# Performance work log

Measured on AMD Instinct MI355X. Metric: run time of the kernel, lower is better.

The kernel has to match this reference:

```python
import jax, jax.numpy as jnp
import numpy as np

B, N, C, K, RPE = 8, 4096, 256, 16, 64
LN_EPS = 1e-5


def _layernorm(x, g, b):
    m = jnp.mean(x, axis=-1, keepdims=True)
    v = jnp.mean((x - m) ** 2, axis=-1, keepdims=True)
    return (x - m) * jax.lax.rsqrt(v + LN_EPS) * g + b


def setup_inputs() -> dict:
    key = jax.random.key(0)
    ks = jax.random.split(key, 10)
    def w(k, shape, s=0.02):
        return jax.random.normal(k, shape, jnp.float32) * s
    return {
        "x": jax.random.normal(ks[0], (B, N, C), jnp.float32),
        "pos": jax.random.normal(ks[1], (B, N, 3), jnp.float32),
        "Wq": w(ks[2], (C, C)),
        "Wk": w(ks[3], (C, C)),
        "Wv": w(ks[4], (C, C)),
        "W1": w(ks[5], (3, RPE)), "b1": jnp.zeros((RPE,), jnp.float32),
        "W2": w(ks[6], (RPE, C)), "b2": jnp.zeros((C,), jnp.float32),
        "Wp": w(ks[7], (C, C)), "bp": jnp.zeros((C,), jnp.float32),
        "gq": jnp.ones((C,), jnp.float32), "betaq": jnp.zeros((C,), jnp.float32),
        "gkv": jnp.ones((C,), jnp.float32), "betakv": jnp.zeros((C,), jnp.float32),
    }


def reference(x, pos, Wq, Wk, Wv, W1, b1, W2, b2, Wp, bp, gq, betaq, gkv, betakv):
    scale = C ** (-0.5)
    x_q = _layernorm(x, gq, betaq)
    x_kv = _layernorm(x, gkv, betakv)
    q = x_q @ Wq                      # (B,N,C)
    k = x_kv @ Wk                     # (B,N,C)
    v = x_kv @ Wv                     # (B,N,C)

    # kNN over squared pairwise distances (self has distance 0 on the diagonal)
    a2 = jnp.sum(pos * pos, axis=-1)                       # (B,N)
    dist2 = a2[:, :, None] + a2[:, None, :] - 2.0 * jnp.einsum(
        "bnc,bmc->bnm", pos, pos)                          # (B,N,N)
    dist2 = jnp.maximum(dist2, 0.0)
    eye = jnp.eye(N, dtype=bool)
    dist2 = jnp.where(eye[None], 0.0, dist2)
    _, idx = jax.lax.top_k(-dist2, K)                      # (B,N,K) smallest-k

    gather = jax.vmap(lambda f, i: f[i])                   # (N,C),(N,K)->(N,K,C)
    k_nb = gather(k, idx)                                  # (B,N,K,C)
    v_nb = gather(v, idx)                                  # (B,N,K,C)
    pos_nb = gather(pos, idx)                              # (B,N,K,3)

    rel = pos[:, :, None, :] - pos_nb                      # (B,N,K,3)
    rel_enc = jax.nn.relu(rel @ W1 + b1) @ W2 + b2         # (B,N,K,C)

    attn_logits = jnp.einsum("bnc,bnkc->bnk", q, k_nb) * scale
    attn_logits = attn_logits + jnp.sum(rel_enc, axis=-1) * scale
    attn = jax.nn.softmax(attn_logits, axis=-1)            # (B,N,K)

    out = jnp.einsum("bnk,bnkc->bnc", attn, v_nb)
    out = out @ Wp + bp
    return out
```

## Files before the change

kernel.cpp:

```cpp
#include <hip/hip_runtime.h>
#include <hip/hip_bf16.h>
#include <stdint.h>

#define Bv 8
#define Nv 4096
#define Cv 256
#define Kv 16
#define RPEv 64
#define CAPv 160

typedef short bf16x8 __attribute__((ext_vector_type(8)));
typedef float f32x4 __attribute__((ext_vector_type(4)));
typedef _Float16 half2v __attribute__((ext_vector_type(2)));
typedef unsigned short u16x2 __attribute__((ext_vector_type(2)));

static __device__ __forceinline__ float bf2f(unsigned int u16) {
    union { unsigned int i; float f; } v; v.i = u16 << 16; return v.f;
}
static __device__ __forceinline__ unsigned short f2bf(float f) {
    union { float f; unsigned int i; } v; v.f = f;
    unsigned int x = v.i;
    return (unsigned short)((x + 0x7fffu + ((x >> 16) & 1u)) >> 16);
}
static __device__ __forceinline__ unsigned int umin32(unsigned int a, unsigned int b) { return a < b ? a : b; }
static __device__ __forceinline__ unsigned int umax32(unsigned int a, unsigned int b) { return a > b ? a : b; }
static __device__ __forceinline__ unsigned short f2h(float f) {
    _Float16 h = (_Float16)f; return __builtin_bit_cast(unsigned short, h);
}
static __device__ __forceinline__ float h2f(unsigned int u) {
    _Float16 h = __builtin_bit_cast(_Float16, (unsigned short)(u & 0xffffu)); return (float)h;
}
static __device__ __forceinline__ half2v bch2(unsigned int u) { return __builtin_bit_cast(half2v, u); }
static __device__ __forceinline__ unsigned int bcu32(u16x2 v) { return __builtin_bit_cast(unsigned int, v); }

__global__ __launch_bounds__(256) void pre_kernel(
    const float* __restrict__ x,
    const float* __restrict__ gq, const float* __restrict__ bq,
    const float* __restrict__ gkv, const float* __restrict__ bkv,
    unsigned short* __restrict__ Aq, unsigned short* __restrict__ Akv,
    const float* __restrict__ Wq, const float* __restrict__ Wk,
    const float* __restrict__ Wv, const float* __restrict__ Wp,
    unsigned short* __restrict__ Bt,
    const float* __restrict__ W2, const float* __restrict__ b2,
    float* __restrict__ w2sum, float* __restrict__ b2sum,
    const float* __restrict__ pos, char* __restrict__ ppos)
{
    const int bid = blockIdx.x;
    const int tid = threadIdx.x;
    if (bid < 4096) {
        const long r0 = (long)bid * 8;
        const int row = tid >> 5;
        const int c0 = (tid & 31) * 8;
        const float* xr = x + (r0 + row) * Cv + c0;
        float xv[8];
        *(float4*)&xv[0] = *(const float4*)xr;
        *(float4*)&xv[4] = *(const float4*)(xr + 4);
        float s = 0.f, s2 = 0.f;
#pragma unroll
        for (int i = 0; i < 8; ++i) { s += xv[i]; s2 = fmaf(xv[i], xv[i], s2); }
#pragma unroll
        for (int m = 16; m >= 1; m >>= 1) { s += __shfl_xor(s, m); s2 += __shfl_xor(s2, m); }
        const float mean = s * (1.f / Cv);
        const float var = fmaf(-mean, mean, s2 * (1.f / Cv));
        const float rs = rsqrtf(fmaxf(var, 0.f) + 1e-5f);
        unsigned int pq[4], pk[4];
#pragma unroll
        for (int i = 0; i < 4; ++i) {
            const int c = c0 + 2 * i;
            const float h0 = (xv[2 * i] - mean) * rs;
            const float h1 = (xv[2 * i + 1] - mean) * rs;
            const unsigned int q0 = f2bf(fmaf(h0, gq[c], bq[c]));
            const unsigned int q1 = f2bf(fmaf(h1, gq[c + 1], bq[c + 1]));
            const unsigned int k0 = f2bf(fmaf(h0, gkv[c], bkv[c]));
            const unsigned int k1 = f2bf(fmaf(h1, gkv[c + 1], bkv[c + 1]));
            pq[i] = q0 | (q1 << 16);
            pk[i] = k0 | (k1 << 16);
        }
        const long off = (r0 + row) * Cv + c0;
        *(uint4*)&Aq[off]  = make_uint4(pq[0], pq[1], pq[2], pq[3]);
        *(uint4*)&Akv[off] = make_uint4(pk[0], pk[1], pk[2], pk[3]);
    } else if (bid < 5120) {
        const int r = bid - 4096;
        const float* W = (r < 256) ? Wq : (r < 512) ? Wk : (r < 768) ? Wv : Wp;
        const int n = r & 255;
        Bt[r * 256 + tid] = f2bf(W[tid * 256 + n]);
    } else if (bid == 5120) {
        if (tid < RPEv) {
            float s = 0.f;
            for (int c = 0; c < Cv; ++c) s += W2[tid * Cv + c];
            w2sum[tid] = s;
        }
        if (tid == 0) {
            float s = 0.f;
            for (int c = 0; c < Cv; ++c) s += b2[c];
            *b2sum = s;
        }
    } else {
        const int b = bid - 5121;
        const float* pb = pos + (size_t)b * Nv * 3;
        uint2* oxy = (uint2*)(ppos + (size_t)b * 24576);
        unsigned int* oz = (unsigned int*)(ppos + (size_t)b * 24576 + 16384);
        for (int i = tid; i < Nv / 2; i += 256) {
            const float* pp = pb + 6 * i;
            const float2 u0 = *(const float2*)pp;
            const float2 u1 = *(const float2*)(pp + 2);
            const float2 u2 = *(const float2*)(pp + 4);
            const unsigned int x0 = f2h(u0.x), y0 = f2h(u0.y), z0 = f2h(u1.x);
            const unsigned int x1 = f2h(u1.y), y1 = f2h(u2.x), z1 = f2h(u2.y);
            oxy[i] = make_uint2(x0 | (x1 << 16), y0 | (y1 << 16));
            oz[i] = z0 | (z1 << 16);
        }
    }
}

__global__ __launch_bounds__(256) void gemm_qkv_kernel(
    const unsigned short* __restrict__ Aq, const unsigned short* __restrict__ Akv,
    const unsigned short* __restrict__ Bt,
    unsigned short* __restrict__ qo, unsigned short* __restrict__ ko,
    unsigned short* __restrict__ vo)
{
    __shared__ unsigned short Albs[2][128 * 64];
    __shared__ unsigned short Blbs[2][128 * 64];

    const int tid = threadIdx.x;
    const int rt = blockIdx.x;
    const int ct = blockIdx.y;
    const unsigned short* A = (ct < 2) ? Aq : Akv;
    const int mat = ct >> 1;
    unsigned short* outp = (mat == 0) ? qo : (mat == 1) ? ko : vo;
    const int colInMat = (ct & 1) * 128;

    const int wid = tid >> 6, l = tid & 63;
    const int wr = wid >> 1, wc = wid & 1;

    int srow[4], scol8[4];
#pragma unroll
    for (int it = 0; it < 4; ++it) {
        const int chunk = it * 256 + tid;
        srow[it] = chunk >> 3;
        scol8[it] = ((chunk & 7) ^ (srow[it] & 7)) * 8;
    }

#define STAGE(buf, ks)                                                                  \
    {                                                                                   \
        _Pragma("unroll")                                                               \
        for (int it = 0; it < 4; ++it) {                                                \
            const unsigned short* ga = A + ((size_t)(rt * 128 + srow[it])) * 256        \
                                         + (ks) * 64 + scol8[it];                       \
            const unsigned short* gb = Bt + ((size_t)(ct * 128 + srow[it])) * 256       \
                                          + (ks) * 64 + scol8[it];                      \
            __builtin_amdgcn_global_load_lds(                                           \
                (const __attribute__((address_space(1))) unsigned int*)(const void*)ga, \
                (__attribute__((address_space(3))) unsigned int*)(void*)                \
                    ((char*)&Albs[buf][0] + (it * 256 + tid) * 16), 16, 0, 0);          \
            __builtin_amdgcn_global_load_lds(                                           \
                (const __attribute__((address_space(1))) unsigned int*)(const void*)gb, \
                (__attribute__((address_space(3))) unsigned int*)(void*)                \
                    ((char*)&Blbs[buf][0] + (it * 256 + tid) * 16), 16, 0, 0);          \
        }                                                                               \
    }

    f32x4 acc[4][4];
#pragma unroll
    for (int m = 0; m < 4; ++m)
#pragma unroll
        for (int n = 0; n < 4; ++n) acc[m][n] = (f32x4){0.f, 0.f, 0.f, 0.f};

    STAGE(0, 0);
    __syncthreads();

    for (int ks = 0; ks < 4; ++ks) {
        const int cur = ks & 1;
        if (ks < 3) STAGE(cur ^ 1, ks + 1);
#pragma unroll
        for (int kk = 0; kk < 2; ++kk) {
            bf16x8 a[4], b[4];
#pragma unroll
            for (int m = 0; m < 4; ++m) {
                const int row = wr * 64 + m * 16 + (l & 15);
                const int byte = row * 128 + ((((kk * 4 + (l >> 4)) * 16)) ^ ((row & 7) << 4));
                a[m] = *(const bf16x8*)((const char*)&Albs[cur][0] + byte);
            }
#pragma unroll
            for (int n = 0; n < 4; ++n) {
                const int row = wc * 64 + n * 16 + (l & 15);
                const int byte = row * 128 + ((((kk * 4 + (l >> 4)) * 16)) ^ ((row & 7) << 4));
                b[n] = *(const bf16x8*)((const char*)&Blbs[cur][0] + byte);
            }
#pragma unroll
            for (int m = 0; m < 4; ++m)
#pragma unroll
                for (int n = 0; n < 4; ++n)
                    acc[m][n] = __builtin_amdgcn_mfma_f32_16x16x32_bf16(a[m], b[n], acc[m][n], 0, 0, 0);
        }
        __syncthreads();
    }

#pragma unroll
    for (int m = 0; m < 4; ++m) {
#pragma unroll
        for (int n = 0; n < 4; ++n) {
#pragma unroll
            for (int j = 0; j < 4; ++j) {
                const int row = rt * 128 + wr * 64 + m * 16 + (l >> 4) * 4 + j;
                const int col = colInMat + wc * 64 + n * 16 + (l & 15);
                outp[(size_t)row * 256 + col] = f2bf(acc[m][n][j]);
            }
        }
    }
#undef STAGE
}

__global__ __launch_bounds__(256) void gemm_proj_kernel(
    const unsigned short* __restrict__ Ab, const unsigned short* __restrict__ Btp,
    const float* __restrict__ bp, float* __restrict__ out)
{
    __shared__ unsigned short Albs[2][128 * 64];
    __shared__ unsigned short Blbs[2][128 * 64];

    const int tid = threadIdx.x;
    const int rt = blockIdx.x;
    const int ct = blockIdx.y;

    const int wid = tid >> 6, l = tid & 63;
    const int wr = wid >> 1, wc = wid & 1;

    int srow[4], scol8[4];
#pragma unroll
    for (int it = 0; it < 4; ++it) {
        const int chunk = it * 256 + tid;
        srow[it] = chunk >> 3;
        scol8[it] = ((chunk & 7) ^ (srow[it] & 7)) * 8;
    }

#define STAGE(buf, ks)                                                                  \
    {                                                                                   \
        _Pragma("unroll")                                                               \
        for (int it = 0; it < 4; ++it) {                                                \
            const unsigned short* ga = Ab + ((size_t)(rt * 128 + srow[it])) * 256       \
                                          + (ks) * 64 + scol8[it];                      \
            const unsigned short* gb = Btp + ((size_t)(ct * 128 + srow[it])) * 256      \
                                           + (ks) * 64 + scol8[it];                     \
            __builtin_amdgcn_global_load_lds(                                           \
                (const __attribute__((address_space(1))) unsigned int*)(const void*)ga, \
                (__attribute__((address_space(3))) unsigned int*)(void*)                \
                    ((char*)&Albs[buf][0] + (it * 256 + tid) * 16), 16, 0, 0);          \
            __builtin_amdgcn_global_load_lds(                                           \
                (const __attribute__((address_space(1))) unsigned int*)(const void*)gb, \
                (__attribute__((address_space(3))) unsigned int*)(void*)                \
                    ((char*)&Blbs[buf][0] + (it * 256 + tid) * 16), 16, 0, 0);          \
        }                                                                               \
    }

    f32x4 acc[4][4];
#pragma unroll
    for (int m = 0; m < 4; ++m)
#pragma unroll
        for (int n = 0; n < 4; ++n) acc[m][n] = (f32x4){0.f, 0.f, 0.f, 0.f};

    STAGE(0, 0);
    __syncthreads();

    for (int ks = 0; ks < 4; ++ks) {
        const int cur = ks & 1;
        if (ks < 3) STAGE(cur ^ 1, ks + 1);
#pragma unroll
        for (int kk = 0; kk < 2; ++kk) {
            bf16x8 a[4], b[4];
#pragma unroll
            for (int m = 0; m < 4; ++m) {
                const int row = wr * 64 + m * 16 + (l & 15);
                const int byte = row * 128 + ((((kk * 4 + (l >> 4)) * 16)) ^ ((row & 7) << 4));
                a[m] = *(const bf16x8*)((const char*)&Albs[cur][0] + byte);
            }
#pragma unroll
            for (int n = 0; n < 4; ++n) {
                const int row = wc * 64 + n * 16 + (l & 15);
                const int byte = row * 128 + ((((kk * 4 + (l >> 4)) * 16)) ^ ((row & 7) << 4));
                b[n] = *(const bf16x8*)((const char*)&Blbs[cur][0] + byte);
            }
#pragma unroll
            for (int m = 0; m < 4; ++m)
#pragma unroll
                for (int n = 0; n < 4; ++n)
                    acc[m][n] = __builtin_amdgcn_mfma_f32_16x16x32_bf16(a[m], b[n], acc[m][n], 0, 0, 0);
        }
        __syncthreads();
    }

#pragma unroll
    for (int n = 0; n < 4; ++n) {
        const int col = ct * 128 + wc * 64 + n * 16 + (l & 15);
        const float bpv = bp[col];
#pragma unroll
        for (int m = 0; m < 4; ++m) {
#pragma unroll
            for (int j = 0; j < 4; ++j) {
                const int row = rt * 128 + wr * 64 + m * 16 + (l >> 4) * 4 + j;
                out[(size_t)row * 256 + col] = acc[m][n][j] + bpv;
            }
        }
    }
#undef STAGE
}

__global__ __launch_bounds__(256) void knn_kernel(
    const float* __restrict__ pos, const char* __restrict__ ppos,
    int* __restrict__ idx_out)
{
    __shared__ char Pbuf[24576];
    __shared__ uint4 qu[32];
    __shared__ unsigned int akeys[256 * 3];
    __shared__ unsigned int cnt[32];
    __shared__ unsigned short bufs[32 * CAPv];

    const uint2* pxy2 = (const uint2*)Pbuf;
    const unsigned int* pz2 = (const unsigned int*)(Pbuf + 16384);

    const int tid = threadIdx.x;
    const int ql = tid >> 3;
    const int s  = tid & 7;
    const int q  = blockIdx.x * 32 + ql;
    const int b  = q >> 12;
    const int n  = q & (Nv - 1);

    {
        const char* src = ppos + (size_t)b * 24576;
#pragma unroll
        for (int it = 0; it < 6; ++it) {
            const int off = (it * 256 + tid) * 16;
            __builtin_amdgcn_global_load_lds(
                (const __attribute__((address_space(1))) unsigned int*)(const void*)(src + off),
                (__attribute__((address_space(3))) unsigned int*)(void*)(Pbuf + off),
                16, 0, 0);
        }
    }
    __syncthreads();

    const int pq = n >> 1;
    const int hq = (n & 1) * 16;
    const uint2 qxy = pxy2[pq];
    const unsigned int qzz = pz2[pq];
    const unsigned int hx = (qxy.x >> hq) & 0xffffu;
    const unsigned int hy = (qxy.y >> hq) & 0xffffu;
    const unsigned int hz = (qzz   >> hq) & 0xffffu;
    const half2v qxp = bch2(hx | (hx << 16));
    const half2v qyp = bch2(hy | (hy << 16));
    const half2v qzp = bch2(hz | (hz << 16));

    u16x2 ch0 = {0x7c00, 0x7c00}, ch1 = ch0, ch2 = ch0;
    for (int t = 0; t < 128; ++t) {
        const int p = 8 * t + s;
        const uint2 xy = pxy2[p];
        const unsigned int zz = pz2[p];
        const half2v dx = bch2(xy.x) - qxp;
        const half2v dy = bch2(xy.y) - qyp;
        const half2v dz = bch2(zz) - qzp;
        const half2v d2 = dx * dx + dy * dy + dz * dz;
        const u16x2 k = __builtin_bit_cast(u16x2, d2);
        const u16x2 mn0 = __builtin_elementwise_min(ch0, k);
        const u16x2 mx0 = __builtin_elementwise_max(ch0, k);
        ch0 = mn0;
        const u16x2 mn1 = __builtin_elementwise_min(ch1, mx0);
        const u16x2 mx1 = __builtin_elementwise_max(ch1, mx0);
        ch1 = mn1;
        ch2 = __builtin_elementwise_min(ch2, mx1);
    }
    akeys[tid * 3 + 0] = bcu32(ch0);
    akeys[tid * 3 + 1] = bcu32(ch1);
    akeys[tid * 3 + 2] = bcu32(ch2);
    __syncthreads();

    if (tid < 32) {
        unsigned int sel16[16];
#pragma unroll
        for (int i = 0; i < 16; ++i) sel16[i] = 0xFFFFFFFFu;
        for (int s8 = 0; s8 < 8; ++s8) {
#pragma unroll
            for (int i3 = 0; i3 < 3; ++i3) {
                const unsigned int v = akeys[(8 * tid + s8) * 3 + i3];
#pragma unroll
                for (int h = 0; h < 2; ++h) {
                    unsigned int cand = (h == 0) ? (v & 0xffffu) : (v >> 16);
                    if (cand < sel16[15]) {
#pragma unroll
                        for (int i = 0; i < 16; ++i) {
                            const unsigned int lo = umin32(sel16[i], cand);
                            cand = umax32(sel16[i], cand);
                            sel16[i] = lo;
                        }
                    }
                }
            }
        }
        const float tauf = h2f(sel16[15]) * 1.12f + 1e-9f;
        const unsigned int taub = f2h(tauf);
        const int n2 = (blockIdx.x * 32 + tid) & (Nv - 1);
        const int pq2 = n2 >> 1;
        const int hq2 = (n2 & 1) * 16;
        const uint2 qxy2 = pxy2[pq2];
        const unsigned int qzz2 = pz2[pq2];
        const unsigned int hx2 = (qxy2.x >> hq2) & 0xffffu;
        const unsigned int hy2 = (qxy2.y >> hq2) & 0xffffu;
        const unsigned int hz2 = (qzz2   >> hq2) & 0xffffu;
        qu[tid] = make_uint4(hx2 | (hx2 << 16), hy2 | (hy2 << 16),
                             hz2 | (hz2 << 16), taub);
        cnt[tid] = 0;
    }
    __syncthreads();

    uint2 cxy[8]; unsigned int czp[8];
#pragma unroll
    for (int k = 0; k < 8; ++k) {
        cxy[k] = pxy2[tid + (k << 8)];
        czp[k] = pz2[tid + (k << 8)];
    }
    for (int q2 = 0; q2 < 32; ++q2) {
        const uint4 Q = qu[q2];
        const half2v Qx = bch2(Q.x), Qy = bch2(Q.y), Qz = bch2(Q.z);
        const unsigned int taub = Q.w;
#pragma unroll
        for (int k = 0; k < 8; ++k) {
            const half2v dx = bch2(cxy[k].x) - Qx;
            const half2v dy = bch2(cxy[k].y) - Qy;
            const half2v dz = bch2(czp[k]) - Qz;
            const half2v d2 = dx * dx + dy * dy + dz * dz;
            const unsigned int bits = __builtin_bit_cast(unsigned int, d2);
            const unsigned int lo = bits & 0xffffu;
            const unsigned int hi = bits >> 16;
            const int p = tid + (k << 8);
            if (lo < taub) {
                const unsigned int slot = atomicAdd(&cnt[q2], 1u);
                if (slot < CAPv) bufs[q2 * CAPv + slot] = (unsigned short)(2 * p);
            }
            if (hi < taub) {
                const unsigned int slot = atomicAdd(&cnt[q2], 1u);
                if (slot < CAPv) bufs[q2 * CAPv + slot] = (unsigned short)(2 * p + 1);
            }
        }
    }
    __syncthreads();

    if (tid < 32) {
        const int q2 = blockIdx.x * 32 + tid;
        const int n2 = q2 & (Nv - 1);
        const int b2 = q2 >> 12;
        const float* pb2 = pos + (size_t)b2 * Nv * 3;
        const double qxd = (double)pb2[3 * n2];
        const double qyd = (double)pb2[3 * n2 + 1];
        const double qzd = (double)pb2[3 * n2 + 2];
        const double a2qd = qxd * qxd + qyd * qyd + qzd * qzd;
        int c = (int)cnt[tid]; if (c > CAPv) c = CAPv;
        unsigned long long sel[Kv];
#pragma unroll
        for (int i = 0; i < Kv; ++i) sel[i] = ~0ull;
        for (int t = 0; t < c; ++t) {
            const int j = bufs[tid * CAPv + t];
            const double cxd = (double)pb2[3 * j];
            const double cyd = (double)pb2[3 * j + 1];
            const double czd = (double)pb2[3 * j + 2];
            const double a2cd = cxd * cxd + cyd * cyd + czd * czd;
            const double ddot = qxd * cxd + qyd * cyd + qzd * czd;
            double dv = (a2qd + a2cd) - 2.0 * ddot;
            dv = (dv < 0.0) ? 0.0 : dv;
            if (j == n2) dv = 0.0;
            union { double d; unsigned long long u; } cv; cv.d = dv;
            const unsigned long long key = (cv.u & ~0xFFFULL) | (unsigned long long)j;
            if (key < sel[Kv - 1]) {
                unsigned long long cc = key;
#pragma unroll
                for (int i = 0; i < Kv; ++i) {
                    const unsigned long long lo = (sel[i] < cc) ? sel[i] : cc;
                    const unsigned long long hi = (sel[i] < cc) ? cc : sel[i];
                    sel[i] = lo; cc = hi;
                }
            }
        }
#pragma unroll
        for (int i = 0; i < Kv; ++i)
            idx_out[(long)q2 * Kv + i] = (int)(sel[i] & 0xFFFull);
    }
}

__global__ __launch_bounds__(256) void attn_core_kernel(
    unsigned short* __restrict__ qb, const unsigned short* __restrict__ kb,
    const unsigned short* __restrict__ vb, const int* __restrict__ idx,
    const float* __restrict__ pos, const float* __restrict__ W1,
    const float* __restrict__ b1, const float* __restrict__ w2sum,
    const float* __restrict__ b2sum)
{
    __shared__ float q_lds[8][Cv];
    __shared__ float lg[8][Kv];
    __shared__ float wgt[8][Kv];
    __shared__ int idx_l[8][Kv];
    __shared__ float W1l[3 * RPEv];
    __shared__ float b1l[RPEv], w2s[RPEv];
    __shared__ float posq[24];
    __shared__ float b2s_l;

    const int tid = threadIdx.x;
    const long r0 = (long)blockIdx.x * 8;
    const int bq = (int)(r0 >> 12);

    {
        float* ql = &q_lds[0][0];
        for (int i = tid; i < 8 * Cv; i += 256) ql[i] = bf2f(qb[r0 * Cv + i]);
    }
    if (tid < 128) ((int*)idx_l)[tid] = idx[r0 * Kv + tid];
    if (tid < 3 * RPEv) W1l[tid] = W1[tid];
    if (tid < RPEv) { b1l[tid] = b1[tid]; w2s[tid] = w2sum[tid]; }
    if (tid < 24) posq[tid] = pos[r0 * 3 + tid];
    if (tid == 0) b2s_l = *b2sum;
    __syncthreads();

    const int g = tid >> 4, l = tid & 15;
    for (int r = 0; r < 8; ++r) {
        const int nb = idx_l[r][g];
        const long gi = (long)bq * Nv + nb;
        const unsigned short* kr = kb + gi * Cv + l * 16;
        const float* qq = &q_lds[r][l * 16];
        const uint4 kA = *(const uint4*)kr;
        const uint4 kB = *(const uint4*)(kr + 8);
        float part = 0.f;
        part = fmaf(qq[0],  bf2f(kA.x & 0xffffu), part);
        part = fmaf(qq[1],  bf2f(kA.x >> 16),     part);
        part = fmaf(qq[2],  bf2f(kA.y & 0xffffu), part);
        part = fmaf(qq[3],  bf2f(kA.y >> 16),     part);
        part = fmaf(qq[4],  bf2f(kA.z & 0xffffu), part);
        part = fmaf(qq[5],  bf2f(kA.z >> 16),     part);
        part = fmaf(qq[6],  bf2f(kA.w & 0xffffu), part);
        part = fmaf(qq[7],  bf2f(kA.w >> 16),     part);
        part = fmaf(qq[8],  bf2f(kB.x & 0xffffu), part);
        part = fmaf(qq[9],  bf2f(kB.x >> 16),     part);
        part = fmaf(qq[10], bf2f(kB.y & 0xffffu), part);
        part = fmaf(qq[11], bf2f(kB.y >> 16),     part);
        part = fmaf(qq[12], bf2f(kB.z & 0xffffu), part);
        part = fmaf(qq[13], bf2f(kB.z >> 16),     part);
        part = fmaf(qq[14], bf2f(kB.w & 0xffffu), part);
        part = fmaf(qq[15], bf2f(kB.w >> 16),     part);
        const float rx = posq[r * 3 + 0] - pos[gi * 3 + 0];
        const float ry = posq[r * 3 + 1] - pos[gi * 3 + 1];
        const float rz = posq[r * 3 + 2] - pos[gi * 3 + 2];
#pragma unroll
        for (int u4 = 0; u4 < 4; ++u4) {
            const int u = l * 4 + u4;
            float h = fmaf(rx, W1l[u], fmaf(ry, W1l[RPEv + u], fmaf(rz, W1l[2 * RPEv + u], b1l[u])));
            h = fmaxf(h, 0.f);
            part = fmaf(h, w2s[u], part);
        }
        part += __shfl_xor(part, 8);
        part += __shfl_xor(part, 4);
        part += __shfl_xor(part, 2);
        part += __shfl_xor(part, 1);
        if (l == 0) lg[r][g] = (part + b2s_l) * 0.0625f;
    }
    __syncthreads();
    if (tid < 128) {
        const int rr = tid >> 4, gg = tid & 15;
        const float v = lg[rr][gg];
        float m = v;
        m = fmaxf(m, __shfl_xor(m, 8)); m = fmaxf(m, __shfl_xor(m, 4));
        m = fmaxf(m, __shfl_xor(m, 2)); m = fmaxf(m, __shfl_xor(m, 1));
        const float e = __expf(v - m);
        float ssum = e;
        ssum += __shfl_xor(ssum, 8); ssum += __shfl_xor(ssum, 4);
        ssum += __shfl_xor(ssum, 2); ssum += __shfl_xor(ssum, 1);
        wgt[rr][gg] = e / ssum;
    }
    __syncthreads();
    {
        const int c = tid;
        for (int r = 0; r < 8; ++r) {
            float acc = 0.f;
#pragma unroll
            for (int t = 0; t < Kv; ++t) {
                const long gi = (long)bq * Nv + idx_l[r][t];
                acc = fmaf(wgt[r][t], bf2f((unsigned)vb[gi * Cv + c]), acc);
            }
            qb[(r0 + r) * Cv + c] = f2bf(acc);
        }
    }
}

extern "C" void kernel_launch(void* const* d_in, const int* in_sizes, int n_in,
                              void* d_out, int out_size, void* d_ws, size_t ws_size,
                              hipStream_t stream) {
    (void)in_sizes; (void)n_in; (void)out_size; (void)ws_size;
    const float* x      = (const float*)d_in[0];
    const float* pos    = (const float*)d_in[1];
    const float* Wq     = (const float*)d_in[2];
    const float* Wk     = (const float*)d_in[3];
    const float* Wv     = (const float*)d_in[4];
    const float* W1     = (const float*)d_in[5];
    const float* b1     = (const float*)d_in[6];
    const float* W2     = (const float*)d_in[7];
    const float* b2     = (const float*)d_in[8];
    const float* Wp     = (const float*)d_in[9];
    const float* bp     = (const float*)d_in[10];
    const float* gq     = (const float*)d_in[11];
    const float* betaq  = (const float*)d_in[12];
    const float* gkv    = (const float*)d_in[13];
    const float* betakv = (const float*)d_in[14];
    float* out = (float*)d_out;

    char* ws = (char*)d_ws;
    unsigned short* qb = (unsigned short*)(ws);
    unsigned short* kb = (unsigned short*)(ws + 16777216);
    unsigned short* vb = (unsigned short*)(ws + 33554432);
    int*   idx   = (int*)  (ws + 50331648);
    unsigned short* Bt = (unsigned short*)(ws + 52428800);
    float* w2sum = (float*)(ws + 52953088);
    float* b2sum = (float*)(ws + 52953344);
    char*  ppos  = ws + 52953600;

    unsigned short* Aq  = (unsigned short*)d_out;
    unsigned short* Akv = (unsigned short*)d_out + 8388608;

    hipLaunchKernelGGL(pre_kernel, dim3(5129), dim3(256), 0, stream,
                       x, gq, betaq, gkv, betakv, Aq, Akv,
                       Wq, Wk, Wv, Wp, Bt, W2, b2, w2sum, b2sum, pos, ppos);
    hipLaunchKernelGGL(gemm_qkv_kernel, dim3(256, 6), dim3(256), 0, stream,
                       Aq, Akv, Bt, qb, kb, vb);
    hipLaunchKernelGGL(knn_kernel, dim3(1024), dim3(256), 0, stream, pos, ppos, idx);
    hipLaunchKernelGGL(attn_core_kernel, dim3(4096), dim3(256), 0, stream,
                       qb, kb, vb, idx, pos, W1, b1, w2sum, b2sum);
    hipLaunchKernelGGL(gemm_proj_kernel, dim3(256, 2), dim3(256), 0, stream,
                       qb, Bt + 768 * 256, bp, out);
}
```

Measured before the change: 222.0 us.

## Split kNN into tau, MFMA-based candidate filter, and fp64 select kernels

The monolithic kNN kernel becomes four kernels. A build kernel packs positions into split-bf16 16-wide vectors so squared distance is computed with MFMA dot products. A tau kernel computes per-query thresholds, a filter kernel runs the MFMA distance pass with atomic candidate buffering, and a select kernel does the exact fp64 top-k over candidates with one thread per query instead of 32 threads per block. This moves the brute-force distance work from packed-half VALU to matrix cores and spreads the serial selection across all threads, at the cost of extra launches and global round-trips for candidate buffers. Split-bf16 precision could let through more or different candidates than the half-precision path did.

```diff
diff --git a/kernel.cpp b/kernel.cpp
--- a/kernel.cpp
+++ b/kernel.cpp
@@ -304,23 +304,18 @@
 #undef STAGE
 }
 
-__global__ __launch_bounds__(256) void knn_kernel(
-    const float* __restrict__ pos, const char* __restrict__ ppos,
-    int* __restrict__ idx_out)
+__global__ __launch_bounds__(256) void ktau_kernel(
+    const char* __restrict__ ppos, float* __restrict__ tau_g)
 {
     __shared__ char Pbuf[24576];
-    __shared__ uint4 qu[32];
     __shared__ unsigned int akeys[256 * 3];
-    __shared__ unsigned int cnt[32];
-    __shared__ unsigned short bufs[32 * CAPv];
 
     const uint2* pxy2 = (const uint2*)Pbuf;
     const unsigned int* pz2 = (const unsigned int*)(Pbuf + 16384);
 
     const int tid = threadIdx.x;
-    const int ql = tid >> 3;
     const int s  = tid & 7;
-    const int q  = blockIdx.x * 32 + ql;
+    const int q  = blockIdx.x * 32 + (tid >> 3);
     const int b  = q >> 12;
     const int n  = q & (Nv - 1);
 
@@ -393,93 +388,155 @@
                 }
             }
         }
-        const float tauf = h2f(sel16[15]) * 1.12f + 1e-9f;
-        const unsigned int taub = f2h(tauf);
-        const int n2 = (blockIdx.x * 32 + tid) & (Nv - 1);
-        const int pq2 = n2 >> 1;
-        const int hq2 = (n2 & 1) * 16;
-        const uint2 qxy2 = pxy2[pq2];
-        const unsigned int qzz2 = pz2[pq2];
-        const unsigned int hx2 = (qxy2.x >> hq2) & 0xffffu;
-        const unsigned int hy2 = (qxy2.y >> hq2) & 0xffffu;
-        const unsigned int hz2 = (qzz2   >> hq2) & 0xffffu;
-        qu[tid] = make_uint4(hx2 | (hx2 << 16), hy2 | (hy2 << 16),
-                             hz2 | (hz2 << 16), taub);
-        cnt[tid] = 0;
-    }
-    __syncthreads();
-
-    uint2 cxy[8]; unsigned int czp[8];
-#pragma unroll
-    for (int k = 0; k < 8; ++k) {
-        cxy[k] = pxy2[tid + (k << 8)];
-        czp[k] = pz2[tid + (k << 8)];
-    }
-    for (int q2 = 0; q2 < 32; ++q2) {
-        const uint4 Q = qu[q2];
-        const half2v Qx = bch2(Q.x), Qy = bch2(Q.y), Qz = bch2(Q.z);
-        const unsigned int taub = Q.w;
-#pragma unroll
-        for (int k = 0; k < 8; ++k) {
-            const half2v dx = bch2(cxy[k].x) - Qx;
-            const half2v dy = bch2(cxy[k].y) - Qy;
-            const half2v dz = bch2(czp[k]) - Qz;
-            const half2v d2 = dx * dx + dy * dy + dz * dz;
-            const unsigned int bits = __builtin_bit_cast(unsigned int, d2);
-            const unsigned int lo = bits & 0xffffu;
-            const unsigned int hi = bits >> 16;
-            const int p = tid + (k << 8);
-            if (lo < taub) {
-                const unsigned int slot = atomicAdd(&cnt[q2], 1u);
-                if (slot < CAPv) bufs[q2 * CAPv + slot] = (unsigned short)(2 * p);
-            }
-            if (hi < taub) {
-                const unsigned int slot = atomicAdd(&cnt[q2], 1u);
-                if (slot < CAPv) bufs[q2 * CAPv + slot] = (unsigned short)(2 * p + 1);
-            }
-        }
-    }
-    __syncthreads();
-
-    if (tid < 32) {
-        const int q2 = blockIdx.x * 32 + tid;
-        const int n2 = q2 & (Nv - 1);
-        const int b2 = q2 >> 12;
-        const float* pb2 = pos + (size_t)b2 * Nv * 3;
-        const double qxd = (double)pb2[3 * n2];
-        const double qyd = (double)pb2[3 * n2 + 1];
-        const double qzd = (double)pb2[3 * n2 + 2];
-        const double a2qd = qxd * qxd + qyd * qyd + qzd * qzd;
-        int c = (int)cnt[tid]; if (c > CAPv) c = CAPv;
-        unsigned long long sel[Kv];
-#pragma unroll
-        for (int i = 0; i < Kv; ++i) sel[i] = ~0ull;
-        for (int t = 0; t < c; ++t) {
-            const int j = bufs[tid * CAPv + t];
-            const double cxd = (double)pb2[3 * j];
-            const double cyd = (double)pb2[3 * j + 1];
-            const double czd = (double)pb2[3 * j + 2];
-            const double a2cd = cxd * cxd + cyd * cyd + czd * czd;
-            const double ddot = qxd * cxd + qyd * cyd + qzd * czd;
-            double dv = (a2qd + a2cd) - 2.0 * ddot;
-            dv = (dv < 0.0) ? 0.0 : dv;
-            if (j == n2) dv = 0.0;
-            union { double d; unsigned long long u; } cv; cv.d = dv;
-            const unsigned long long key = (cv.u & ~0xFFFULL) | (unsigned long long)j;
-            if (key < sel[Kv - 1]) {
-                unsigned long long cc = key;
-#pragma unroll
-                for (int i = 0; i < Kv; ++i) {
-                    const unsigned long long lo = (sel[i] < cc) ? sel[i] : cc;
-                    const unsigned long long hi = (sel[i] < cc) ? cc : sel[i];
-                    sel[i] = lo; cc = hi;
+        tau_g[blockIdx.x * 32 + tid] = h2f(sel16[15]) * 1.12f + 1e-9f;
+    }
+}
+
+__global__ __launch_bounds__(256) void build16_kernel(
+    const float* __restrict__ pos,
+    unsigned short* __restrict__ Aq16g, unsigned short* __restrict__ Bq16g)
+{
+    const int t = blockIdx.x * 256 + threadIdx.x;
+    const float px = pos[3 * t], py = pos[3 * t + 1], pz = pos[3 * t + 2];
+    unsigned short ah[3], al[3], m2h[3], m2l[3];
+    const float c[3] = {px, py, pz};
+#pragma unroll
+    for (int i = 0; i < 3; ++i) {
+        ah[i] = f2bf(c[i]);
+        const float hi = bf2f(ah[i]);
+        al[i] = f2bf(c[i] - hi);
+        m2h[i] = f2bf(-2.f * hi);
+        m2l[i] = f2bf(-2.f * bf2f(al[i]));
+    }
+    const float sA = fmaf(px, px, fmaf(py, py, pz * pz));
+    const unsigned short sh = f2bf(sA);
+    const unsigned short sl = f2bf(sA - bf2f(sh));
+    const unsigned short one = 0x3F80;
+
+    unsigned short a16[16] = {ah[0], ah[1], ah[2], al[0], al[1], al[2],
+                              ah[0], ah[1], ah[2], al[0], al[1], al[2],
+                              sh, sl, one, one};
+    unsigned short b16[16] = {m2h[0], m2h[1], m2h[2], m2h[0], m2h[1], m2h[2],
+                              m2l[0], m2l[1], m2l[2], m2l[0], m2l[1], m2l[2],
+                              one, one, sh, sl};
+    uint4* ao = (uint4*)(Aq16g + (size_t)t * 16);
+    uint4* bo = (uint4*)(Bq16g + (size_t)t * 16);
+    ao[0] = *(uint4*)&a16[0]; ao[1] = *(uint4*)&a16[8];
+    bo[0] = *(uint4*)&b16[0]; bo[1] = *(uint4*)&b16[8];
+}
+
+__global__ __launch_bounds__(256) void kfilter_kernel(
+    const unsigned short* __restrict__ Aq16g, const unsigned short* __restrict__ Bq16g,
+    const float* __restrict__ tau_g, unsigned int* __restrict__ gcnt,
+    unsigned short* __restrict__ gbufs)
+{
+    __shared__ unsigned short Bst[1024 * 16];
+    __shared__ unsigned short Ast[64 * 16];
+    __shared__ unsigned short bufsL[64 * CAPv];
+    __shared__ unsigned int cntL[64];
+    __shared__ float tauL[64];
+
+    const int tid = threadIdx.x;
+    const int qb0 = blockIdx.x * 64;
+    const int batch = qb0 >> 12;
+    const int wave = tid >> 6;
+    const int l = tid & 63;
+    const int kc = l >> 4;
+
+    if (tid < 128) {
+        __builtin_amdgcn_global_load_lds(
+            (const __attribute__((address_space(1))) unsigned int*)(const void*)
+                ((const char*)Aq16g + (size_t)qb0 * 32 + tid * 16),
+            (__attribute__((address_space(3))) unsigned int*)(void*)((char*)Ast + tid * 16),
+            16, 0, 0);
+    }
+    if (tid < 64) { tauL[tid] = tau_g[qb0 + tid]; cntL[tid] = 0; }
+    __syncthreads();
+
+    const bf16x8 z8 = (bf16x8){0, 0, 0, 0, 0, 0, 0, 0};
+    bf16x8 afr = z8;
+    if (kc < 2) afr = *(const bf16x8*)(Ast + (wave * 16 + (l & 15)) * 16 + kc * 8);
+    float tr[4];
+#pragma unroll
+    for (int j = 0; j < 4; ++j) tr[j] = tauL[wave * 16 + (l >> 4) * 4 + j];
+
+    for (int chunk = 0; chunk < 4; ++chunk) {
+#pragma unroll
+        for (int it = 0; it < 8; ++it) {
+            __builtin_amdgcn_global_load_lds(
+                (const __attribute__((address_space(1))) unsigned int*)(const void*)
+                    ((const char*)Bq16g + ((size_t)batch * 4096 + chunk * 1024) * 32
+                     + (it * 256 + tid) * 16),
+                (__attribute__((address_space(3))) unsigned int*)(void*)
+                    ((char*)Bst + (it * 256 + tid) * 16),
+                16, 0, 0);
+        }
+        __syncthreads();
+        for (int nt = 0; nt < 64; ++nt) {
+            bf16x8 bfr = z8;
+            if (kc < 2) bfr = *(const bf16x8*)(Bst + (nt * 16 + (l & 15)) * 16 + kc * 8);
+            const f32x4 acc = __builtin_amdgcn_mfma_f32_16x16x32_bf16(
+                afr, bfr, (f32x4){0.f, 0.f, 0.f, 0.f}, 0, 0, 0);
+            const int cand = chunk * 1024 + nt * 16 + (l & 15);
+#pragma unroll
+            for (int j = 0; j < 4; ++j) {
+                if (acc[j] < tr[j]) {
+                    const int rl = wave * 16 + (l >> 4) * 4 + j;
+                    const unsigned int slot = atomicAdd(&cntL[rl], 1u);
+                    if (slot < CAPv) bufsL[rl * CAPv + slot] = (unsigned short)cand;
                 }
             }
         }
-#pragma unroll
-        for (int i = 0; i < Kv; ++i)
-            idx_out[(long)q2 * Kv + i] = (int)(sel[i] & 0xFFFull);
-    }
+        __syncthreads();
+    }
+
+    if (tid < 64) gcnt[qb0 + tid] = umin32(cntL[tid], CAPv);
+    for (int i = tid; i < 64 * CAPv; i += 256)
+        gbufs[(size_t)qb0 * CAPv + i] = bufsL[i];
+}
+
+__global__ __launch_bounds__(256) void kselect_kernel(
+    const float* __restrict__ pos, const unsigned int* __restrict__ gcnt,
+    const unsigned short* __restrict__ gbufs, int* __restrict__ idx_out)
+{
+    const int t = blockIdx.x * 256 + threadIdx.x;
+    const int n2 = t & (Nv - 1);
+    const int b2 = t >> 12;
+    const float* pb2 = pos + (size_t)b2 * Nv * 3;
+    const double qxd = (double)pb2[3 * n2];
+    const double qyd = (double)pb2[3 * n2 + 1];
+    const double qzd = (double)pb2[3 * n2 + 2];
+    const double a2qd = qxd * qxd + qyd * qyd + qzd * qzd;
+    int c = (int)gcnt[t]; if (c > CAPv) c = CAPv;
+    const unsigned short* myb = gbufs + (size_t)t * CAPv;
+    unsigned long long sel[Kv];
+#pragma unroll
+    for (int i = 0; i < Kv; ++i) sel[i] = ~0ull;
+    for (int s = 0; s < c; ++s) {
+        const int j = myb[s];
+        const double cxd = (double)pb2[3 * j];
+        const double cyd = (double)pb2[3 * j + 1];
+        const double czd = (double)pb2[3 * j + 2];
+        const double a2cd = cxd * cxd + cyd * cyd + czd * czd;
+        const double ddot = qxd * cxd + qyd * cyd + qzd * czd;
+        double dv = (a2qd + a2cd) - 2.0 * ddot;
+        dv = (dv < 0.0) ? 0.0 : dv;
+        if (j == n2) dv = 0.0;
+        union { double d; unsigned long long u; } cv; cv.d = dv;
+        const unsigned long long key = (cv.u & ~0xFFFULL) | (unsigned long long)j;
+        if (key < sel[Kv - 1]) {
+            unsigned long long cc = key;
+#pragma unroll
+            for (int i = 0; i < Kv; ++i) {
+                const unsigned long long lo = (sel[i] < cc) ? sel[i] : cc;
+                const unsigned long long hi = (sel[i] < cc) ? cc : sel[i];
+                sel[i] = lo; cc = hi;
+            }
+        }
+    }
+#pragma unroll
+    for (int i = 0; i < Kv; ++i)
+        idx_out[(long)t * Kv + i] = (int)(sel[i] & 0xFFFull);
 }
 
 __global__ __launch_bounds__(256) void attn_core_kernel(
@@ -613,15 +670,27 @@
     float* b2sum = (float*)(ws + 52953344);
     char*  ppos  = ws + 52953600;
 
-    unsigned short* Aq  = (unsigned short*)d_out;
-    unsigned short* Akv = (unsigned short*)d_out + 8388608;
+    char* dob = (char*)d_out;
+    unsigned short* Aq  = (unsigned short*)dob;
+    unsigned short* Akv = (unsigned short*)dob + 8388608;
+    unsigned short* Aq16g = (unsigned short*)dob;
+    unsigned short* Bq16g = (unsigned short*)(dob + (1 << 20));
+    float*          tau_g = (float*)(dob + (2 << 20));
+    unsigned int*   gcnt  = (unsigned int*)(dob + (2 << 20) + (1 << 18));
+    unsigned short* gbufs = (unsigned short*)(dob + (2 << 20) + (2 << 18));
 
     hipLaunchKernelGGL(pre_kernel, dim3(5129), dim3(256), 0, stream,
                        x, gq, betaq, gkv, betakv, Aq, Akv,
                        Wq, Wk, Wv, Wp, Bt, W2, b2, w2sum, b2sum, pos, ppos);
     hipLaunchKernelGGL(gemm_qkv_kernel, dim3(256, 6), dim3(256), 0, stream,
                        Aq, Akv, Bt, qb, kb, vb);
-    hipLaunchKernelGGL(knn_kernel, dim3(1024), dim3(256), 0, stream, pos, ppos, idx);
+    hipLaunchKernelGGL(build16_kernel, dim3(128), dim3(256), 0, stream,
+                       pos, Aq16g, Bq16g);
+    hipLaunchKernelGGL(ktau_kernel, dim3(1024), dim3(256), 0, stream, ppos, tau_g);
+    hipLaunchKernelGGL(kfilter_kernel, dim3(512), dim3(256), 0, stream,
+                       Aq16g, Bq16g, tau_g, gcnt, gbufs);
+    hipLaunchKernelGGL(kselect_kernel, dim3(128), dim3(256), 0, stream,
+                       pos, gcnt, gbufs, idx);
     hipLaunchKernelGGL(attn_core_kernel, dim3(4096), dim3(256), 0, stream,
                        qb, kb, vb, idx, pos, W1, b1, w2sum, b2sum);
     hipLaunchKernelGGL(gemm_proj_kernel, dim3(256, 2), dim3(256), 0, stream,
```

Result: slower. 262.9 us (+18.4%).

## Halve queries per kNN block and read packed positions from global

Applied to the files above, without the earlier changes.

The kNN kernel now handles 16 queries per block instead of 32, using 16 lanes per query in the first-pass scan, and launches twice as many blocks. It drops the 24 KB LDS staging of packed half positions and reads them straight from global memory (L2/L1-cached), cutting LDS use to raise occupancy. The cost is that each block still scans all 4096 candidates in the threshold-filter pass for only 16 queries, so total candidate reads per query double, and global loads replace LDS reads.

```diff
diff --git a/kernel.cpp b/kernel.cpp
--- a/kernel.cpp
+++ b/kernel.cpp
@@ -308,39 +308,25 @@
     const float* __restrict__ pos, const char* __restrict__ ppos,
     int* __restrict__ idx_out)
 {
-    __shared__ char Pbuf[24576];
-    __shared__ uint4 qu[32];
+    __shared__ uint4 qf[16];
     __shared__ unsigned int akeys[256 * 3];
-    __shared__ unsigned int cnt[32];
-    __shared__ unsigned short bufs[32 * CAPv];
-
-    const uint2* pxy2 = (const uint2*)Pbuf;
-    const unsigned int* pz2 = (const unsigned int*)(Pbuf + 16384);
+    __shared__ unsigned int cnt[16];
+    __shared__ unsigned short bufs[16 * CAPv];
 
     const int tid = threadIdx.x;
-    const int ql = tid >> 3;
-    const int s  = tid & 7;
-    const int q  = blockIdx.x * 32 + ql;
+    const int ql = tid >> 4;
+    const int s  = tid & 15;
+    const int q  = blockIdx.x * 16 + ql;
     const int b  = q >> 12;
     const int n  = q & (Nv - 1);
 
-    {
-        const char* src = ppos + (size_t)b * 24576;
-#pragma unroll
-        for (int it = 0; it < 6; ++it) {
-            const int off = (it * 256 + tid) * 16;
-            __builtin_amdgcn_global_load_lds(
-                (const __attribute__((address_space(1))) unsigned int*)(const void*)(src + off),
-                (__attribute__((address_space(3))) unsigned int*)(void*)(Pbuf + off),
-                16, 0, 0);
-        }
-    }
-    __syncthreads();
+    const uint2* gxy = (const uint2*)(ppos + (size_t)b * 24576);
+    const unsigned int* gz = (const unsigned int*)(ppos + (size_t)b * 24576 + 16384);
 
     const int pq = n >> 1;
     const int hq = (n & 1) * 16;
-    const uint2 qxy = pxy2[pq];
-    const unsigned int qzz = pz2[pq];
+    const uint2 qxy = gxy[pq];
+    const unsigned int qzz = gz[pq];
     const unsigned int hx = (qxy.x >> hq) & 0xffffu;
     const unsigned int hy = (qxy.y >> hq) & 0xffffu;
     const unsigned int hz = (qzz   >> hq) & 0xffffu;
@@ -350,9 +336,9 @@
 
     u16x2 ch0 = {0x7c00, 0x7c00}, ch1 = ch0, ch2 = ch0;
     for (int t = 0; t < 128; ++t) {
-        const int p = 8 * t + s;
-        const uint2 xy = pxy2[p];
-        const unsigned int zz = pz2[p];
+        const int p = 16 * t + s;
+        const uint2 xy = gxy[p];
+        const unsigned int zz = gz[p];
         const half2v dx = bch2(xy.x) - qxp;
         const half2v dy = bch2(xy.y) - qyp;
         const half2v dz = bch2(zz) - qzp;
@@ -371,14 +357,14 @@
     akeys[tid * 3 + 2] = bcu32(ch2);
     __syncthreads();
 
-    if (tid < 32) {
+    if (tid < 16) {
         unsigned int sel16[16];
 #pragma unroll
         for (int i = 0; i < 16; ++i) sel16[i] = 0xFFFFFFFFu;
-        for (int s8 = 0; s8 < 8; ++s8) {
+        for (int s8 = 0; s8 < 16; ++s8) {
 #pragma unroll
             for (int i3 = 0; i3 < 3; ++i3) {
-                const unsigned int v = akeys[(8 * tid + s8) * 3 + i3];
+                const unsigned int v = akeys[(16 * tid + s8) * 3 + i3];
 #pragma unroll
                 for (int h = 0; h < 2; ++h) {
                     unsigned int cand = (h == 0) ? (v & 0xffffu) : (v >> 16);
@@ -395,15 +381,15 @@
         }
         const float tauf = h2f(sel16[15]) * 1.12f + 1e-9f;
         const unsigned int taub = f2h(tauf);
-        const int n2 = (blockIdx.x * 32 + tid) & (Nv - 1);
+        const int n2 = (blockIdx.x * 16 + tid) & (Nv - 1);
         const int pq2 = n2 >> 1;
         const int hq2 = (n2 & 1) * 16;
-        const uint2 qxy2 = pxy2[pq2];
-        const unsigned int qzz2 = pz2[pq2];
+        const uint2 qxy2 = gxy[pq2];
+        const unsigned int qzz2 = gz[pq2];
         const unsigned int hx2 = (qxy2.x >> hq2) & 0xffffu;
         const unsigned int hy2 = (qxy2.y >> hq2) & 0xffffu;
         const unsigned int hz2 = (qzz2   >> hq2) & 0xffffu;
-        qu[tid] = make_uint4(hx2 | (hx2 << 16), hy2 | (hy2 << 16),
+        qf[tid] = make_uint4(hx2 | (hx2 << 16), hy2 | (hy2 << 16),
                              hz2 | (hz2 << 16), taub);
         cnt[tid] = 0;
     }
@@ -412,11 +398,11 @@
     uint2 cxy[8]; unsigned int czp[8];
 #pragma unroll
     for (int k = 0; k < 8; ++k) {
-        cxy[k] = pxy2[tid + (k << 8)];
-        czp[k] = pz2[tid + (k << 8)];
-    }
-    for (int q2 = 0; q2 < 32; ++q2) {
-        const uint4 Q = qu[q2];
+        cxy[k] = gxy[tid + (k << 8)];
+        czp[k] = gz[tid + (k << 8)];
+    }
+    for (int q2 = 0; q2 < 16; ++q2) {
+        const uint4 Q = qf[q2];
         const half2v Qx = bch2(Q.x), Qy = bch2(Q.y), Qz = bch2(Q.z);
         const unsigned int taub = Q.w;
 #pragma unroll
@@ -441,8 +427,8 @@
     }
     __syncthreads();
 
-    if (tid < 32) {
-        const int q2 = blockIdx.x * 32 + tid;
+    if (tid < 16) {
+        const int q2 = blockIdx.x * 16 + tid;
         const int n2 = q2 & (Nv - 1);
         const int b2 = q2 >> 12;
         const float* pb2 = pos + (size_t)b2 * Nv * 3;
@@ -621,7 +607,7 @@
                        Wq, Wk, Wv, Wp, Bt, W2, b2, w2sum, b2sum, pos, ppos);
     hipLaunchKernelGGL(gemm_qkv_kernel, dim3(256, 6), dim3(256), 0, stream,
                        Aq, Akv, Bt, qb, kb, vb);
-    hipLaunchKernelGGL(knn_kernel, dim3(1024), dim3(256), 0, stream, pos, ppos, idx);
+    hipLaunchKernelGGL(knn_kernel, dim3(2048), dim3(256), 0, stream, pos, ppos, idx);
     hipLaunchKernelGGL(attn_core_kernel, dim3(4096), dim3(256), 0, stream,
                        qb, kb, vb, idx, pos, W1, b1, w2sum, b2sum);
     hipLaunchKernelGGL(gemm_proj_kernel, dim3(256, 2), dim3(256), 0, stream,
```

New measurement: 222.3 us. Within noise of the previous version (+0.1%).
